# Optimization experiments

Hardware: AMD Instinct MI355X
Metric: run time of the kernel (lower is better)

The kernel has to match this reference:

```python
import jax, jax.numpy as jnp
import numpy as np

B, S, D = 4, 1024, 1024
H, DK = 16, 64

def setup_inputs() -> dict:
    key = jax.random.key(0)
    ks = jax.random.split(key, 12)
    s = lambda k, shape, scale: (jax.random.normal(k, shape, dtype=jnp.float32) * scale)
    inp = {
        "query": s(ks[0], (B, S, D), 1.0),
        "key":   s(ks[1], (B, S, D), 1.0),
        "value": s(ks[2], (B, S, D), 1.0),
        # per-head query projections stacked: [H, D, DK]
        "Wq": s(ks[3], (H, D, DK), D ** -0.5),
        "bq": jnp.zeros((H, DK), jnp.float32),
        # shared key / value projections (MQA)
        "Wk": s(ks[4], (D, DK), D ** -0.5),
        "bk": jnp.zeros((DK,), jnp.float32),
        "Wv": s(ks[5], (D, DK), D ** -0.5),
        "bv": jnp.zeros((DK,), jnp.float32),
        # combine_heads: Dense(key_dim) applied to concat of H head outputs
        "Wc": s(ks[6], (H * DK, DK), (H * DK) ** -0.5),
        "bc": jnp.zeros((DK,), jnp.float32),
    }
    return inp


def reference(query, key, value, Wq, bq, Wk, bk, Wv, bv, Wc, bc):
    # per-head query projections, batched over heads: [B,H,S,DK]
    q = jnp.einsum('bsd,hdk->bhsk', query, Wq) + bq[None, :, None, :]
    # shared K/V (multi-query attention): [B,S,DK]
    k = jnp.einsum('bsd,dk->bsk', key, Wk) + bk
    v = jnp.einsum('bsd,dk->bsk', value, Wv) + bv
    scale = 1.0 / jnp.sqrt(jnp.asarray(DK, q.dtype))
    # scores: [B,H,S,S], K broadcast across heads
    scores = jnp.einsum('bhsk,btk->bhst', q, k) * scale
    attn = jax.nn.softmax(scores, axis=-1)
    # head outputs: [B,H,S,DK]
    out_h = jnp.einsum('bhst,btk->bhsk', attn, v)
    # concat heads along last axis (head order preserved): [B,S,H*DK]
    concat = out_h.transpose(0, 2, 1, 3).reshape(B, S, H * DK)
    output = concat @ Wc + bc  # [B,S,DK]; dropout=0.0 -> identity
    return output, attn
```

## Files before the change

kernel.cpp:

```cpp
#include <hip/hip_runtime.h>

typedef __bf16 bf16;
typedef __attribute__((ext_vector_type(4))) float f32x4;
typedef __attribute__((ext_vector_type(8))) bf16 bf16x8;
typedef __attribute__((ext_vector_type(4))) bf16 bf16x4;

constexpr int Bc = 4, Sc = 1024, Dc = 1024, Hc = 16, DKc = 64;
#define ESCALE 0.18033688011112042f
#define EXP2F(x) __builtin_amdgcn_exp2f(x)


__device__ __forceinline__ void stage64(bf16* s, const void* g, int ld, int f32src) {
  const int t = threadIdx.x;
#pragma unroll
  for (int i = 0; i < 2; ++i) {
    const int G = t + i * 256;
    const int r = G >> 3, gr = G & 7;
    bf16x8 o;
    if (f32src) {
      const float* gp = (const float*)g + (long)r * ld + gr * 8;
      const f32x4 a = *(const f32x4*)gp;
      const f32x4 b = *(const f32x4*)(gp + 4);
      o[0]=(bf16)a[0]; o[1]=(bf16)a[1]; o[2]=(bf16)a[2]; o[3]=(bf16)a[3];
      o[4]=(bf16)b[0]; o[5]=(bf16)b[1]; o[6]=(bf16)b[2]; o[7]=(bf16)b[3];
    } else {
      o = *(const bf16x8*)((const bf16*)g + (long)r * ld + gr * 8);
    }
    *(bf16x8*)(s + r * 64 + ((gr * 8) ^ ((r & 7) << 3))) = o;
  }
}

__device__ __forceinline__ bf16x8 frag_ld(const bf16* s, int row, int kofs) {
  const int lane = threadIdx.x & 63;
  const int c0 = kofs + (((lane >> 4) & 3) << 2);
  const int sw = (row & 7) << 3;
  union { bf16x8 v8; bf16x4 v4[2]; } u;
  u.v4[0] = *(const bf16x4*)(s + row * 64 + (c0 ^ sw));
  u.v4[1] = *(const bf16x4*)(s + row * 64 + ((c0 + 16) ^ sw));
  return u.v8;
}

__device__ __forceinline__ void gld16(const bf16* g, bf16* l) {
  __builtin_amdgcn_global_load_lds(
      (const __attribute__((address_space(1))) void*)g,
      (__attribute__((address_space(3))) void*)l, 16, 0, 0);
}

#define WAIT_BAR(vm) do { \
  asm volatile("s_waitcnt vmcnt(" vm ")" ::: "memory"); \
  __builtin_amdgcn_s_barrier(); \
  __builtin_amdgcn_sched_barrier(0); } while (0)

__global__ __launch_bounds__(256) void transpose_weights(
    const float* __restrict__ Wq, const float* __restrict__ Wk,
    const float* __restrict__ Wv, const float* __restrict__ Wc,
    bf16* __restrict__ WqT, bf16* __restrict__ WkT,
    bf16* __restrict__ WvT, bf16* __restrict__ WcT) {
  const int bid = blockIdx.x;
  const float* src; bf16* dst; float scl; int r0;
  if (bid < 256)      { const int hh = bid >> 4; r0 = (bid & 15) * 64;
                        src = Wq + (hh << 16); dst = WqT + (hh << 16); scl = ESCALE; }
  else if (bid < 272) { r0 = (bid - 256) * 64; src = Wk; dst = WkT; scl = 1.f; }
  else if (bid < 288) { r0 = (bid - 272) * 64; src = Wv; dst = WvT; scl = 1.f; }
  else                { r0 = (bid - 288) * 64; src = Wc; dst = WcT; scl = 1.f; }

  __shared__ float tile[64][68];
  const int t = threadIdx.x;
  const int rr = t >> 4, cc = (t & 15) * 4;
#pragma unroll
  for (int i = 0; i < 4; ++i) {
    const f32x4 v = *(const f32x4*)(src + (long)(r0 + rr + i * 16) * 64 + cc);
    *(f32x4*)(&tile[rr + i * 16][cc]) = v;
  }
  __syncthreads();
#pragma unroll
  for (int i = 0; i < 2; ++i) {
    const int g = t + i * 256, orow = g >> 3, oc = (g & 7) * 8;
    bf16x8 o;
#pragma unroll
    for (int jj = 0; jj < 8; ++jj) o[jj] = (bf16)(tile[oc + jj][orow] * scl);
    *(bf16x8*)(dst + (long)orow * 1024 + r0 + oc) = o;
  }
}

__global__ __launch_bounds__(256) void proj_kernel(
    const float* __restrict__ query, const float* __restrict__ key,
    const float* __restrict__ value, const bf16* __restrict__ WqT,
    const bf16* __restrict__ WkT, const bf16* __restrict__ WvT,
    const float* __restrict__ bq, const float* __restrict__ bk,
    const float* __restrict__ bv, bf16* __restrict__ q_cat,
    bf16* __restrict__ k_proj, bf16* __restrict__ vTp) {
  __shared__ bf16 sA[2][8192];
  __shared__ bf16 sB[2][8192];
  const int bid = blockIdx.x;
  const int t = threadIdx.x;
  const int lane = t & 63;
  const int w = t >> 6;

  if (bid < 256) {
    const int m0 = (bid >> 3) << 7, n0 = (bid & 7) << 7;
    const int wr = w >> 1, wc = w & 1;

    f32x4 acc[4][4];
#pragma unroll
    for (int mi = 0; mi < 4; ++mi)
#pragma unroll
      for (int ni = 0; ni < 4; ++ni) acc[mi][ni] = (f32x4){0.f, 0.f, 0.f, 0.f};

    auto sQA = [&](int p, int kk) {
      const int r = t >> 1, ch = (t & 1) << 5;
      const float* gp = query + (long)(m0 + r) * 1024 + kk + ch;
#pragma unroll
      for (int j = 0; j < 4; ++j) {
        const f32x4 a = *(const f32x4*)(gp + j * 8);
        const f32x4 b = *(const f32x4*)(gp + j * 8 + 4);
        bf16x8 o;
        o[0]=(bf16)a[0]; o[1]=(bf16)a[1]; o[2]=(bf16)a[2]; o[3]=(bf16)a[3];
        o[4]=(bf16)b[0]; o[5]=(bf16)b[1]; o[6]=(bf16)b[2]; o[7]=(bf16)b[3];
        *(bf16x8*)(&sA[p][r * 64 + ((ch + j * 8) ^ ((r & 7) << 3))]) = o;
      }
    };
    auto sQB = [&](int p, int kk) {
#pragma unroll
      for (int i = 0; i < 4; ++i) {
        const int G = t + i * 256, r = G >> 3, c8 = (G & 7) << 3;
        const bf16x8 v = *(const bf16x8*)(WqT + (long)(n0 + r) * 1024 + kk + c8);
        *(bf16x8*)(&sB[p][r * 64 + (c8 ^ ((r & 7) << 3))]) = v;
      }
    };

    sQA(0, 0); sQB(0, 0);
    __syncthreads();
    for (int it = 0; it < 16; ++it) {
      const int p = it & 1;
      if (it < 15) { sQA(p ^ 1, (it + 1) * 64); sQB(p ^ 1, (it + 1) * 64); }
#pragma unroll
      for (int ks = 0; ks < 2; ++ks) {
        bf16x8 af[4], bfr[4];
#pragma unroll
        for (int mi = 0; mi < 4; ++mi)
          af[mi] = frag_ld(sA[p], wr * 64 + mi * 16 + (lane & 15), ks * 32);
#pragma unroll
        for (int ni = 0; ni < 4; ++ni)
          bfr[ni] = frag_ld(sB[p], wc * 64 + ni * 16 + (lane & 15), ks * 32);
#pragma unroll
        for (int mi = 0; mi < 4; ++mi)
#pragma unroll
          for (int ni = 0; ni < 4; ++ni)
            acc[mi][ni] = __builtin_amdgcn_mfma_f32_16x16x32_bf16(af[mi], bfr[ni], acc[mi][ni], 0, 0, 0);
      }
      __syncthreads();
    }

    const int rb = m0 + wr * 64 + ((lane >> 4) << 2);
#pragma unroll
    for (int ni = 0; ni < 4; ++ni) {
      const int col = n0 + wc * 64 + ni * 16 + (lane & 15);
      const float bn = bq[col] * ESCALE;
#pragma unroll
      for (int mi = 0; mi < 4; ++mi)
#pragma unroll
        for (int r4 = 0; r4 < 4; ++r4)
          q_cat[(long)(rb + mi * 16 + r4) * 1024 + col] = (bf16)(acc[mi][ni][r4] + bn);
    }
    return;
  }

  const void* A; const void* BT; bf16* C; const float* bias;
  int m0, n0, ldA, ldBT, ldC, aF32, bF32, biasM;
  if (bid < 320) {
    m0 = (bid - 256) << 6; n0 = 0;
    A = key;    ldA = 1024; aF32 = 1;
    BT = WkT;   ldBT = 1024; bF32 = 0;
    C = k_proj; ldC = 64; bias = bk; biasM = 0;
  } else {
    const int j = bid - 320;
    m0 = 0; n0 = (j & 15) << 6;
    A = WvT; ldA = 1024; aF32 = 0;
    BT = value + ((long)(j >> 4) << 20); ldBT = 1024; bF32 = 1;
    C = vTp + ((long)(j >> 4) << 16); ldC = 1024; bias = bv; biasM = 1;
  }

  f32x4 acc[4];
#pragma unroll
  for (int nb = 0; nb < 4; ++nb) acc[nb] = (f32x4){0.f, 0.f, 0.f, 0.f};

  stage64(sA[0], aF32 ? (const void*)((const float*)A + (long)m0 * ldA)
                      : (const void*)((const bf16*)A + (long)m0 * ldA), ldA, aF32);
  stage64(sB[0], bF32 ? (const void*)((const float*)BT + (long)n0 * ldBT)
                      : (const void*)((const bf16*)BT + (long)n0 * ldBT), ldBT, bF32);
  __syncthreads();

  for (int it = 0; it < 16; ++it) {
    const int p = it & 1;
    if (it < 15) {
      const int kk = (it + 1) * 64;
      stage64(sA[p ^ 1], aF32 ? (const void*)((const float*)A + (long)m0 * ldA + kk)
                              : (const void*)((const bf16*)A + (long)m0 * ldA + kk), ldA, aF32);
      stage64(sB[p ^ 1], bF32 ? (const void*)((const float*)BT + (long)n0 * ldBT + kk)
                              : (const void*)((const bf16*)BT + (long)n0 * ldBT + kk), ldBT, bF32);
    }
#pragma unroll
    for (int ks = 0; ks < 2; ++ks) {
      const bf16x8 af = frag_ld(sA[p], 16 * w + (lane & 15), ks * 32);
#pragma unroll
      for (int nb = 0; nb < 4; ++nb) {
        const bf16x8 bfr = frag_ld(sB[p], nb * 16 + (lane & 15), ks * 32);
        acc[nb] = __builtin_amdgcn_mfma_f32_16x16x32_bf16(af, bfr, acc[nb], 0, 0, 0);
      }
    }
    __syncthreads();
  }

  const int rbase = m0 + 16 * w + ((lane >> 4) << 2);
#pragma unroll
  for (int nb = 0; nb < 4; ++nb) {
    const int col = n0 + nb * 16 + (lane & 15);
    const float bn = biasM ? 0.f : bias[col];
#pragma unroll
    for (int r = 0; r < 4; ++r) {
      const int row = rbase + r;
      C[(long)row * ldC + col] = (bf16)(acc[nb][r] + (biasM ? bias[row] : bn));
    }
  }
}

__global__ __launch_bounds__(256) void combine_kernel(
    const bf16* __restrict__ concat, const bf16* __restrict__ WcT,
    float* __restrict__ part) {
  const int ks = blockIdx.x >> 6;
  const int m0 = (blockIdx.x & 63) * 64;
  const int k0 = ks * 256;
  __shared__ bf16 sA[2][4096];
  __shared__ bf16 sB[2][4096];
  const int lane = threadIdx.x & 63;
  const int w = threadIdx.x >> 6;

  f32x4 acc[4];
#pragma unroll
  for (int nb = 0; nb < 4; ++nb) acc[nb] = (f32x4){0.f, 0.f, 0.f, 0.f};

  stage64(sA[0], concat + (long)m0 * 1024 + k0, 1024, 0);
  stage64(sB[0], WcT + k0, 1024, 0);
  __syncthreads();
  for (int it = 0; it < 4; ++it) {
    const int p = it & 1;
    if (it < 3) {
      const int kk = k0 + (it + 1) * 64;
      stage64(sA[p ^ 1], concat + (long)m0 * 1024 + kk, 1024, 0);
      stage64(sB[p ^ 1], WcT + kk, 1024, 0);
    }
#pragma unroll
    for (int ksl = 0; ksl < 2; ++ksl) {
      const bf16x8 af = frag_ld(sA[p], 16 * w + (lane & 15), ksl * 32);
#pragma unroll
      for (int nb = 0; nb < 4; ++nb) {
        const bf16x8 bfr = frag_ld(sB[p], nb * 16 + (lane & 15), ksl * 32);
        acc[nb] = __builtin_amdgcn_mfma_f32_16x16x32_bf16(af, bfr, acc[nb], 0, 0, 0);
      }
    }
    __syncthreads();
  }
  const int rbase = m0 + 16 * w + ((lane >> 4) << 2);
  float* pb = part + (long)ks * 262144;
#pragma unroll
  for (int nb = 0; nb < 4; ++nb) {
    const int col = nb * 16 + (lane & 15);
#pragma unroll
    for (int r = 0; r < 4; ++r)
      pb[(long)(rbase + r) * 64 + col] = acc[nb][r];
  }
}

__global__ __launch_bounds__(256) void reduce_combine(
    const float* __restrict__ part, const float* __restrict__ bc,
    float* __restrict__ out0) {
  const int i = blockIdx.x * 256 + threadIdx.x;
  out0[i] = part[i] + part[i + 262144] + part[i + 524288] + part[i + 786432]
          + bc[i & 63];
}

__global__ __launch_bounds__(128, 4) void attn_kernel(
    const bf16* __restrict__ q_cat, const bf16* __restrict__ k_proj,
    const bf16* __restrict__ vT, float* __restrict__ attn_out,
    bf16* __restrict__ concat) {
  const int s0 = blockIdx.x * 64;
  const int h = blockIdx.y, b = blockIdx.z;
  const int t = threadIdx.x;
  const int lane = t & 63;
  const int w = t >> 6;

  __shared__ bf16 sK[2][4096];
  __shared__ bf16 sV[2][4096];

  const bf16* kp = k_proj + (long)b * Sc * DKc;
  const bf16* vp = vT + (long)b * DKc * Sc;
  float* ao = attn_out + ((long)(b * Hc + h) * Sc + s0) * Sc;
  bf16* co = concat + (long)(b * Sc + s0) * (Hc * DKc) + h * DKc;

  const int c0q = (lane >> 4) << 2;
  const int wq0 = w * 32;

  const int rloc = t >> 3;
  const int col8 = ((t & 7) ^ (rloc & 7)) << 3;
  const int ldsw = w << 9;

  auto stageK = [&](int pb, int tt) {
#pragma unroll
    for (int c = 0; c < 4; ++c)
      gld16(kp + ((long)tt << 12) + (c * 16 + rloc) * 64 + col8,
            &sK[pb][c * 1024 + ldsw]);
  };
  auto stageV = [&](int pb, int tt) {
#pragma unroll
    for (int c = 0; c < 4; ++c)
      gld16(vp + (long)(c * 16 + rloc) * 1024 + tt * 64 + col8,
            &sV[pb][c * 1024 + ldsw]);
  };

  bf16x8 qf[2][2];
#pragma unroll
  for (int qg = 0; qg < 2; ++qg) {
    const bf16* qrow = q_cat + (long)(b * Sc + s0 + wq0 + qg * 16 + (lane & 15)) * 1024 + h * 64;
    union { bf16x8 v8; bf16x4 v4[2]; } a, c;
    a.v4[0] = *(const bf16x4*)(qrow + c0q);
    a.v4[1] = *(const bf16x4*)(qrow + c0q + 16);
    c.v4[0] = *(const bf16x4*)(qrow + c0q + 32);
    c.v4[1] = *(const bf16x4*)(qrow + c0q + 48);
    qf[qg][0] = a.v8; qf[qg][1] = c.v8;
  }

  stageK(0, 0);
  WAIT_BAR("0");
  float lsum[2] = {0.f, 0.f};
  for (int tc = 0; tc < 16; ++tc) {
    const int p = tc & 1;
    if (tc < 15) stageK(p ^ 1, tc + 1);
    bf16x8 kf[2][4];
#pragma unroll
    for (int ks = 0; ks < 2; ++ks)
#pragma unroll
      for (int nb = 0; nb < 4; ++nb)
        kf[ks][nb] = frag_ld(sK[p], nb * 16 + (lane & 15), ks * 32);
#pragma unroll
    for (int qg = 0; qg < 2; ++qg) {
      f32x4 sc[4];
#pragma unroll
      for (int nb = 0; nb < 4; ++nb) sc[nb] = (f32x4){0.f, 0.f, 0.f, 0.f};
#pragma unroll
      for (int ks = 0; ks < 2; ++ks)
#pragma unroll
        for (int nb = 0; nb < 4; ++nb)
          sc[nb] = __builtin_amdgcn_mfma_f32_16x16x32_bf16(kf[ks][nb], qf[qg][ks], sc[nb], 0, 0, 0);
#pragma unroll
      for (int nb = 0; nb < 4; ++nb)
#pragma unroll
        for (int r = 0; r < 4; ++r) lsum[qg] += EXP2F(sc[nb][r]);
    }
    if (tc < 15) WAIT_BAR("0");
  }

#pragma unroll
  for (int qg = 0; qg < 2; ++qg) {
    lsum[qg] += __shfl_xor(lsum[qg], 16, 64);
    lsum[qg] += __shfl_xor(lsum[qg], 32, 64);
  }
  const float invl0 = 1.f / lsum[0], invl1 = 1.f / lsum[1];

  f32x4 oacc[2][4];
#pragma unroll
  for (int qg = 0; qg < 2; ++qg)
#pragma unroll
    for (int nb = 0; nb < 4; ++nb) oacc[qg][nb] = (f32x4){0.f, 0.f, 0.f, 0.f};

  stageK(0, 0);
  stageV(0, 0);
  WAIT_BAR("0");
  for (int tc = 0; tc < 16; ++tc) {
    const int p = tc & 1;
    if (tc < 15) { stageK(p ^ 1, tc + 1); stageV(p ^ 1, tc + 1); }
    bf16x8 kf[2][4];
#pragma unroll
    for (int ks = 0; ks < 2; ++ks)
#pragma unroll
      for (int nb = 0; nb < 4; ++nb)
        kf[ks][nb] = frag_ld(sK[p], nb * 16 + (lane & 15), ks * 32);
    bf16x8 pa[2][2];
#pragma unroll
    for (int qg = 0; qg < 2; ++qg) {
      f32x4 sc[4];
#pragma unroll
      for (int nb = 0; nb < 4; ++nb) sc[nb] = (f32x4){0.f, 0.f, 0.f, 0.f};
#pragma unroll
      for (int ks = 0; ks < 2; ++ks)
#pragma unroll
        for (int nb = 0; nb < 4; ++nb)
          sc[nb] = __builtin_amdgcn_mfma_f32_16x16x32_bf16(kf[ks][nb], qf[qg][ks], sc[nb], 0, 0, 0);
      const float invl = qg ? invl1 : invl0;
      float* aobase = ao + (long)(wq0 + qg * 16 + (lane & 15)) * Sc + tc * 64 + c0q;
      float e[4][4];
#pragma unroll
      for (int nb = 0; nb < 4; ++nb) {
#pragma unroll
        for (int r = 0; r < 4; ++r) e[nb][r] = EXP2F(sc[nb][r]);
        f32x4 av;
#pragma unroll
        for (int r = 0; r < 4; ++r) av[r] = e[nb][r] * invl;
        *(f32x4*)(aobase + nb * 16) = av;
      }
#pragma unroll
      for (int ks = 0; ks < 2; ++ks)
#pragma unroll
        for (int jj = 0; jj < 4; ++jj) {
          pa[qg][ks][jj]     = (bf16)e[2 * ks][jj];
          pa[qg][ks][4 + jj] = (bf16)e[2 * ks + 1][jj];
        }
    }
#pragma unroll
    for (int ks = 0; ks < 2; ++ks)
#pragma unroll
      for (int nb = 0; nb < 4; ++nb) {
        const bf16x8 vf = frag_ld(sV[p], nb * 16 + (lane & 15), ks * 32);
        oacc[0][nb] = __builtin_amdgcn_mfma_f32_16x16x32_bf16(pa[0][ks], vf, oacc[0][nb], 0, 0, 0);
        oacc[1][nb] = __builtin_amdgcn_mfma_f32_16x16x32_bf16(pa[1][ks], vf, oacc[1][nb], 0, 0, 0);
      }
    if (tc < 15) WAIT_BAR("8");
  }

#pragma unroll
  for (int qg = 0; qg < 2; ++qg) {
    const float invl = qg ? invl1 : invl0;
    float invo[4];
#pragma unroll
    for (int r = 0; r < 4; ++r) invo[r] = __shfl(invl, c0q + r, 64);
#pragma unroll
    for (int nb = 0; nb < 4; ++nb) {
#pragma unroll
      for (int r = 0; r < 4; ++r) {
        const int row = wq0 + qg * 16 + c0q + r;
        const int col = nb * 16 + (lane & 15);
        co[(long)row * (Hc * DKc) + col] = (bf16)(oacc[qg][nb][r] * invo[r]);
      }
    }
  }
}


extern "C" void kernel_launch(void* const* d_in, const int* in_sizes, int n_in,
                              void* d_out, int out_size, void* d_ws, size_t ws_size,
                              hipStream_t stream) {
  const float* query = (const float*)d_in[0];
  const float* key   = (const float*)d_in[1];
  const float* value = (const float*)d_in[2];
  const float* Wq = (const float*)d_in[3];
  const float* bq = (const float*)d_in[4];
  const float* Wk = (const float*)d_in[5];
  const float* bk = (const float*)d_in[6];
  const float* Wv = (const float*)d_in[7];
  const float* bv = (const float*)d_in[8];
  const float* Wc = (const float*)d_in[9];
  const float* bc = (const float*)d_in[10];

  bf16* WqT    = (bf16*)d_ws;
  bf16* WkT    = WqT + 1048576;
  bf16* WvT    = WkT + 65536;
  bf16* WcT    = WvT + 65536;
  bf16* q_cat  = WcT + 65536;
  bf16* k_proj = q_cat + 4194304;
  bf16* vTp    = k_proj + 262144;
  bf16* concat = vTp + 262144;
  float* part  = (float*)(concat + 4194304);

  float* out0 = (float*)d_out;
  float* attn = out0 + (long)Bc * Sc * DKc;

  transpose_weights<<<304, 256, 0, stream>>>(Wq, Wk, Wv, Wc, WqT, WkT, WvT, WcT);

  proj_kernel<<<384, 256, 0, stream>>>(query, key, value, WqT, WkT, WvT,
                                       bq, bk, bv, q_cat, k_proj, vTp);

  attn_kernel<<<dim3(16, 16, 4), 128, 0, stream>>>(q_cat, k_proj, vTp, attn, concat);

  combine_kernel<<<256, 256, 0, stream>>>(concat, WcT, part);
  reduce_combine<<<1024, 256, 0, stream>>>(part, bc, out0);
}
```

Before: 160.3 us.

## Keep full per-batch K resident in LDS and share it across two heads per block

The attention kernel now uses 512-thread blocks covering 128 query rows and two heads. All 16 K tiles (128 KB) are loaded into LDS once and reused for both the softmax-sum pass and the output pass, instead of being streamed twice. V is streamed through a 3-deep ring buffer with tuned vmcnt waits. The goal is to cut redundant K/V global loads and barriers. In exchange, occupancy drops to one large block per CU, and the grid shrinks to 256 blocks.

```diff
diff --git a/kernel.cpp b/kernel.cpp
--- a/kernel.cpp
+++ b/kernel.cpp
@@ -280,18 +280,20 @@
           + bc[i & 63];
 }
 
-__global__ __launch_bounds__(128, 4) void attn_kernel(
+__global__ __launch_bounds__(512, 1) void attn_kernel(
     const bf16* __restrict__ q_cat, const bf16* __restrict__ k_proj,
     const bf16* __restrict__ vT, float* __restrict__ attn_out,
     bf16* __restrict__ concat) {
-  const int s0 = blockIdx.x * 64;
-  const int h = blockIdx.y, b = blockIdx.z;
+  const int s0 = blockIdx.x * 128;
+  const int hp = blockIdx.y, b = blockIdx.z;
   const int t = threadIdx.x;
   const int lane = t & 63;
   const int w = t >> 6;
-
-  __shared__ bf16 sK[2][4096];
-  __shared__ bf16 sV[2][4096];
+  const int h = hp * 2 + (w >> 2);
+  const int wq0 = (w & 3) * 32;
+
+  __shared__ bf16 sK[16][4096];
+  __shared__ bf16 sV[3][4096];
 
   const bf16* kp = k_proj + (long)b * Sc * DKc;
   const bf16* vp = vT + (long)b * DKc * Sc;
@@ -299,23 +301,16 @@
   bf16* co = concat + (long)(b * Sc + s0) * (Hc * DKc) + h * DKc;
 
   const int c0q = (lane >> 4) << 2;
-  const int wq0 = w * 32;
 
   const int rloc = t >> 3;
   const int col8 = ((t & 7) ^ (rloc & 7)) << 3;
   const int ldsw = w << 9;
 
-  auto stageK = [&](int pb, int tt) {
-#pragma unroll
-    for (int c = 0; c < 4; ++c)
-      gld16(kp + ((long)tt << 12) + (c * 16 + rloc) * 64 + col8,
-            &sK[pb][c * 1024 + ldsw]);
+  auto stageK = [&](int tile) {
+    gld16(kp + ((long)tile << 12) + rloc * 64 + col8, &sK[tile][ldsw]);
   };
-  auto stageV = [&](int pb, int tt) {
-#pragma unroll
-    for (int c = 0; c < 4; ++c)
-      gld16(vp + (long)(c * 16 + rloc) * 1024 + tt * 64 + col8,
-            &sV[pb][c * 1024 + ldsw]);
+  auto stageV = [&](int buf, int tile) {
+    gld16(vp + (long)rloc * 1024 + tile * 64 + col8, &sV[buf][ldsw]);
   };
 
   bf16x8 qf[2][2];
@@ -330,18 +325,19 @@
     qf[qg][0] = a.v8; qf[qg][1] = c.v8;
   }
 
-  stageK(0, 0);
-  WAIT_BAR("0");
+#pragma unroll
+  for (int i = 0; i < 16; ++i) stageK(i);
+  stageV(0, 0); stageV(1, 1);
+  WAIT_BAR("2");
+
   float lsum[2] = {0.f, 0.f};
   for (int tc = 0; tc < 16; ++tc) {
-    const int p = tc & 1;
-    if (tc < 15) stageK(p ^ 1, tc + 1);
     bf16x8 kf[2][4];
 #pragma unroll
     for (int ks = 0; ks < 2; ++ks)
 #pragma unroll
       for (int nb = 0; nb < 4; ++nb)
-        kf[ks][nb] = frag_ld(sK[p], nb * 16 + (lane & 15), ks * 32);
+        kf[ks][nb] = frag_ld(&sK[tc][0], nb * 16 + (lane & 15), ks * 32);
 #pragma unroll
     for (int qg = 0; qg < 2; ++qg) {
       f32x4 sc[4];
@@ -357,7 +353,6 @@
 #pragma unroll
         for (int r = 0; r < 4; ++r) lsum[qg] += EXP2F(sc[nb][r]);
     }
-    if (tc < 15) WAIT_BAR("0");
   }
 
 #pragma unroll
@@ -373,18 +368,15 @@
 #pragma unroll
     for (int nb = 0; nb < 4; ++nb) oacc[qg][nb] = (f32x4){0.f, 0.f, 0.f, 0.f};
 
-  stageK(0, 0);
-  stageV(0, 0);
-  WAIT_BAR("0");
+  WAIT_BAR("1");
   for (int tc = 0; tc < 16; ++tc) {
-    const int p = tc & 1;
-    if (tc < 15) { stageK(p ^ 1, tc + 1); stageV(p ^ 1, tc + 1); }
+    if (tc + 2 < 16) stageV((tc + 2) % 3, tc + 2);
     bf16x8 kf[2][4];
 #pragma unroll
     for (int ks = 0; ks < 2; ++ks)
 #pragma unroll
       for (int nb = 0; nb < 4; ++nb)
-        kf[ks][nb] = frag_ld(sK[p], nb * 16 + (lane & 15), ks * 32);
+        kf[ks][nb] = frag_ld(&sK[tc][0], nb * 16 + (lane & 15), ks * 32);
     bf16x8 pa[2][2];
 #pragma unroll
     for (int qg = 0; qg < 2; ++qg) {
@@ -420,11 +412,13 @@
     for (int ks = 0; ks < 2; ++ks)
 #pragma unroll
       for (int nb = 0; nb < 4; ++nb) {
-        const bf16x8 vf = frag_ld(sV[p], nb * 16 + (lane & 15), ks * 32);
+        const bf16x8 vf = frag_ld(&sV[tc % 3][0], nb * 16 + (lane & 15), ks * 32);
         oacc[0][nb] = __builtin_amdgcn_mfma_f32_16x16x32_bf16(pa[0][ks], vf, oacc[0][nb], 0, 0, 0);
         oacc[1][nb] = __builtin_amdgcn_mfma_f32_16x16x32_bf16(pa[1][ks], vf, oacc[1][nb], 0, 0, 0);
       }
-    if (tc < 15) WAIT_BAR("8");
+    if (tc == 0)       WAIT_BAR("9");
+    else if (tc <= 13) WAIT_BAR("17");
+    else if (tc == 14) WAIT_BAR("16");
   }
 
 #pragma unroll
@@ -479,7 +473,7 @@
   proj_kernel<<<384, 256, 0, stream>>>(query, key, value, WqT, WkT, WvT,
                                        bq, bk, bv, q_cat, k_proj, vTp);
 
-  attn_kernel<<<dim3(16, 16, 4), 128, 0, stream>>>(q_cat, k_proj, vTp, attn, concat);
+  attn_kernel<<<dim3(8, 8, 4), 512, 0, stream>>>(q_cat, k_proj, vTp, attn, concat);
 
   combine_kernel<<<256, 256, 0, stream>>>(concat, WcT, part);
   reduce_combine<<<1024, 256, 0, stream>>>(part, bc, out0);
```

After: 170.5 us. +6.4%, slower.
